# Performance work log

Hardware: AMD Instinct MI355X
Metric: run time of the kernel (lower is better)

The kernel has to match this reference:

```python
import jax, jax.numpy as jnp
import numpy as np

D_MODEL = 2048
NUM_HEADS = 16
HEAD_DIM = D_MODEL // NUM_HEADS
D_FF = 8192
EPS = 1e-6


def rmsnorm(x, w):
    return x * jax.lax.rsqrt(jnp.mean(x * x, axis=-1, keepdims=True) + EPS) * w


def setup_inputs() -> dict:
    key = jax.random.key(0)
    ks = jax.random.split(key, 8)
    B, S, D = 2, 2048, D_MODEL
    s = lambda d: 1.0 / np.sqrt(d)
    return {
        "x": jax.random.normal(ks[0], (B, S, D), dtype=jnp.float32),
        "w_qkv": jax.random.normal(ks[1], (D, 3 * D), dtype=jnp.float32) * s(D),
        "w_out": jax.random.normal(ks[2], (D, D), dtype=jnp.float32) * s(D),
        "w1": jax.random.normal(ks[3], (D, D_FF), dtype=jnp.float32) * s(D),
        "w2": jax.random.normal(ks[4], (D_FF, D), dtype=jnp.float32) * s(D_FF),
        "w3": jax.random.normal(ks[5], (D, D_FF), dtype=jnp.float32) * s(D),
        "g1": jnp.ones((D,), dtype=jnp.float32),
        "g2": jnp.ones((D,), dtype=jnp.float32),
    }


def attention(x, w_qkv, w_out):
    B, S, D = x.shape
    H, Hd = NUM_HEADS, HEAD_DIM
    qkv = (x @ w_qkv).reshape(B, S, 3, H, Hd)
    q = qkv[:, :, 0].transpose(0, 2, 1, 3)  # [B,H,S,Hd]
    k = qkv[:, :, 1].transpose(0, 2, 1, 3)
    v = qkv[:, :, 2].transpose(0, 2, 1, 3)
    scale = Hd ** -0.5
    attn = jnp.einsum("bhqd,bhkd->bhqk", q, k) * scale
    causal = jnp.tril(jnp.ones((S, S), dtype=bool))
    attn = jnp.where(causal, attn, -jnp.inf)
    attn = jax.nn.softmax(attn, axis=-1)
    out = jnp.einsum("bhqk,bhkd->bhqd", attn, v)
    out = out.transpose(0, 2, 1, 3).reshape(B, S, D)
    return out @ w_out


def ffn(x, w1, w2, w3):
    return (jax.nn.silu(x @ w1) * (x @ w3)) @ w2


def reference(x, w_qkv, w_out, w1, w2, w3, g1, g2):
    x = x + attention(rmsnorm(x, g1), w_qkv, w_out)
    return x + ffn(rmsnorm(x, g2), w1, w2, w3)
```

## Files before the change

### kernel.cpp

```cpp
#include <hip/hip_runtime.h>
#include <cstdint>
#include <cstddef>

typedef __bf16 bf16x8 __attribute__((ext_vector_type(8)));
typedef float f32x4 __attribute__((ext_vector_type(4)));

__device__ __forceinline__ void gl_lds16(const void* g, void* l) {
  __builtin_amdgcn_global_load_lds(
      (const __attribute__((address_space(1))) void*)g,
      (__attribute__((address_space(3))) void*)l, 16, 0, 0);
}

__global__ __launch_bounds__(256) void wconv_t_k(const float* __restrict__ W,
                                                 __bf16* __restrict__ WT,
                                                 int K, int N) {
  __shared__ float tile[32][33];
  const int c0 = blockIdx.x * 32, r0 = blockIdx.y * 32;
  const int tx = threadIdx.x & 31, ty = threadIdx.x >> 5;
#pragma unroll
  for (int i = 0; i < 32; i += 8)
    tile[ty + i][tx] = W[(size_t)(r0 + ty + i) * N + c0 + tx];
  __syncthreads();
#pragma unroll
  for (int i = 0; i < 32; i += 8)
    WT[(size_t)(c0 + ty + i) * K + r0 + tx] = (__bf16)tile[tx][ty + i];
}

__global__ __launch_bounds__(256) void rmsnorm_k(const float* __restrict__ x,
                                                 const float* __restrict__ g,
                                                 __bf16* __restrict__ out) {
  constexpr int D = 2048;
  const int row = blockIdx.x, t = threadIdx.x;
  const float4* xr = (const float4*)(x + (size_t)row * D);
  float4 a = xr[t * 2], b2 = xr[t * 2 + 1];
  float ss = a.x * a.x + a.y * a.y + a.z * a.z + a.w * a.w +
             b2.x * b2.x + b2.y * b2.y + b2.z * b2.z + b2.w * b2.w;
#pragma unroll
  for (int d = 1; d < 64; d <<= 1) ss += __shfl_xor(ss, d, 64);
  __shared__ float red[4];
  if ((t & 63) == 0) red[t >> 6] = ss;
  __syncthreads();
  float rs = rsqrtf((red[0] + red[1] + red[2] + red[3]) * (1.f / D) + 1e-6f);
  const float4* gr = (const float4*)g;
  float4 ga = gr[t * 2], gb = gr[t * 2 + 1];
  bf16x8 o8;
  o8[0] = (__bf16)(a.x * rs * ga.x);
  o8[1] = (__bf16)(a.y * rs * ga.y);
  o8[2] = (__bf16)(a.z * rs * ga.z);
  o8[3] = (__bf16)(a.w * rs * ga.w);
  o8[4] = (__bf16)(b2.x * rs * gb.x);
  o8[5] = (__bf16)(b2.y * rs * gb.y);
  o8[6] = (__bf16)(b2.z * rs * gb.z);
  o8[7] = (__bf16)(b2.w * rs * gb.w);
  *(bf16x8*)(out + (size_t)row * D + t * 8) = o8;
}

__global__ __launch_bounds__(256) void addrms_k(const float* __restrict__ p0,
                                                const float* __restrict__ p1,
                                                const float* __restrict__ res,
                                                const float* __restrict__ g,
                                                float* __restrict__ hout,
                                                __bf16* __restrict__ xnout) {
  constexpr int D = 2048;
  const int row = blockIdx.x, t = threadIdx.x;
  const size_t base = (size_t)row * D;
  float4 h[2];
#pragma unroll
  for (int j = 0; j < 2; ++j) {
    float4 a = ((const float4*)(p0 + base))[t * 2 + j];
    float4 b = ((const float4*)(p1 + base))[t * 2 + j];
    float4 c = ((const float4*)(res + base))[t * 2 + j];
    h[j].x = a.x + b.x + c.x; h[j].y = a.y + b.y + c.y;
    h[j].z = a.z + b.z + c.z; h[j].w = a.w + b.w + c.w;
    ((float4*)(hout + base))[t * 2 + j] = h[j];
  }
  float ss = h[0].x * h[0].x + h[0].y * h[0].y + h[0].z * h[0].z + h[0].w * h[0].w +
             h[1].x * h[1].x + h[1].y * h[1].y + h[1].z * h[1].z + h[1].w * h[1].w;
#pragma unroll
  for (int d = 1; d < 64; d <<= 1) ss += __shfl_xor(ss, d, 64);
  __shared__ float red[4];
  if ((t & 63) == 0) red[t >> 6] = ss;
  __syncthreads();
  float rs = rsqrtf((red[0] + red[1] + red[2] + red[3]) * (1.f / D) + 1e-6f);
  const float4* gr = (const float4*)g;
  float4 ga = gr[t * 2], gb = gr[t * 2 + 1];
  bf16x8 o8;
  o8[0] = (__bf16)(h[0].x * rs * ga.x);
  o8[1] = (__bf16)(h[0].y * rs * ga.y);
  o8[2] = (__bf16)(h[0].z * rs * ga.z);
  o8[3] = (__bf16)(h[0].w * rs * ga.w);
  o8[4] = (__bf16)(h[1].x * rs * gb.x);
  o8[5] = (__bf16)(h[1].y * rs * gb.y);
  o8[6] = (__bf16)(h[1].z * rs * gb.z);
  o8[7] = (__bf16)(h[1].w * rs * gb.w);
  *(bf16x8*)(xnout + base + t * 8) = o8;
}

__global__ __launch_bounds__(256) void addred_k(const float* __restrict__ p0,
                                                const float* __restrict__ p1,
                                                const float* __restrict__ res,
                                                float* __restrict__ out, int n4) {
  int i = blockIdx.x * 256 + threadIdx.x;
  const int stride = gridDim.x * 256;
  for (; i < n4; i += stride) {
    float4 a = ((const float4*)p0)[i];
    float4 b = ((const float4*)p1)[i];
    float4 c = ((const float4*)res)[i];
    float4 o = {a.x + b.x + c.x, a.y + b.y + c.y, a.z + b.z + c.z, a.w + b.w + c.w};
    ((float4*)out)[i] = o;
  }
}

#define RD_A(BUF, HALF) do {                                        \
  const __bf16* aT_ = &As[BUF][0] + aoff + (HALF) * 4096;           \
  _Pragma("unroll")                                                 \
  for (int mi = 0; mi < 4; ++mi) {                                  \
    Ar[mi][0] = *(const bf16x8*)(aT_ + mi * 1024 + k0off);          \
    Ar[mi][1] = *(const bf16x8*)(aT_ + mi * 1024 + k1off);          \
  } } while (0)

#define RD_B(BUF, NH) do {                                          \
  const __bf16* bT_ = &Bs[BUF][0] + boff + (NH) * 2048;             \
  _Pragma("unroll")                                                 \
  for (int ni = 0; ni < 2; ++ni) {                                  \
    Br[NH][ni][0] = *(const bf16x8*)(bT_ + ni * 1024 + k0off);      \
    Br[NH][ni][1] = *(const bf16x8*)(bT_ + ni * 1024 + k1off);      \
  } } while (0)

#define MQ(MH, NH) do {                                             \
  _Pragma("unroll")                                                 \
  for (int mi = 0; mi < 4; ++mi) {                                  \
    _Pragma("unroll")                                               \
    for (int ni = 0; ni < 2; ++ni) {                                \
      f32x4& a_ = acc[(MH) * 4 + mi][(NH) * 2 + ni];                \
      a_ = __builtin_amdgcn_mfma_f32_16x16x32_bf16(Ar[mi][0], Br[NH][ni][0], a_, 0, 0, 0); \
      a_ = __builtin_amdgcn_mfma_f32_16x16x32_bf16(Ar[mi][1], Br[NH][ni][1], a_, 0, 0, 0); \
    } } } while (0)

#define PH_MID() do {                                               \
  __builtin_amdgcn_sched_barrier(0);                                \
  __builtin_amdgcn_s_barrier();                                     \
  asm volatile("s_waitcnt lgkmcnt(0)" ::: "memory");                \
  __builtin_amdgcn_sched_barrier(0);                                \
  __builtin_amdgcn_s_setprio(1);                                    \
} while (0)

#define PH_END(VM) do {                                             \
  __builtin_amdgcn_s_setprio(0);                                    \
  asm volatile("s_waitcnt vmcnt(" #VM ")" ::: "memory");            \
  __builtin_amdgcn_sched_barrier(0);                                \
  __builtin_amdgcn_s_barrier();                                     \
} while (0)

#define PH_END_NOVM() do {                                          \
  __builtin_amdgcn_s_setprio(0);                                    \
  __builtin_amdgcn_s_barrier();                                     \
} while (0)

#define KTILE(BUF, STG0, STG1, STG2, STG3, END0, END1, END3) do {   \
  RD_A(BUF, 0); RD_B(BUF, 0); STG0; PH_MID(); MQ(0, 0); END0;       \
  RD_B(BUF, 1);               STG1; PH_MID(); MQ(0, 1); END1;       \
  RD_A(BUF, 1);               STG2; PH_MID(); MQ(1, 1); PH_END_NOVM(); \
                              STG3; PH_MID(); MQ(1, 0); END3;       \
} while (0)

template <int MODE>
__global__ __launch_bounds__(512, 2) void gemm8_k(
    const __bf16* __restrict__ A, const __bf16* __restrict__ BT,
    const float* __restrict__ res, const __bf16* __restrict__ aux,
    void* __restrict__ Cout, int M, int N, int K, int lda, int cswz) {
  __shared__ alignas(16) __bf16 As[2][256 * 64];
  __shared__ alignas(16) __bf16 Bs[2][256 * 64];
  const int tid = threadIdx.x;
  const int lane = tid & 63, w = tid >> 6;
  const int wm = w >> 2, wn = w & 3;
  const int l15 = lane & 15, l16 = lane >> 4;

  const int nbx = gridDim.x, nby = gridDim.y;
  const int nwg = nbx * nby;
  const int bid = blockIdx.y * nbx + blockIdx.x;
  const int swz = (bid & 7) * (nwg >> 3) + (bid >> 3);
  int bx, by;
  if (cswz) { by = swz % nby; bx = swz / nby; }
  else      { bx = swz % nbx; by = swz / nbx; }
  const int m0 = by * 256, n0 = bx * 256;
  const int nkt = K >> 6;

  float* CoutF = (float*)Cout;
  if constexpr (MODE == 4) {
    const int z = blockIdx.z;
    A += (size_t)z * K;
    BT += (size_t)z * K;
    CoutF += (size_t)z * M * N;
  }

  const int srow = tid >> 3;
  const int scole = ((tid & 7) * 8) ^ ((srow & 7) << 3);
  const int brow_i = ((tid >> 8) << 6) + ((tid >> 3) & 31);

  auto stgA = [&](int t, int h) {
    if (t < nkt) {
      char* dst = (char*)(&As[t & 1][0]) + h * 8192 + tid * 16;
      const __bf16* src = A + (size_t)(m0 + h * 64 + srow) * lda + t * 64 + scole;
      gl_lds16(src, dst);
      gl_lds16(src + (size_t)128 * lda, dst + 16384);
    }
  };
  auto stgB = [&](int t, int h) {
    if (t < nkt) {
      const int r = h * 32 + brow_i;
      char* dst = (char*)(&Bs[t & 1][0]) + r * 128 + (tid & 7) * 16;
      const __bf16* src = BT + (size_t)(n0 + r) * lda + t * 64 + scole;
      gl_lds16(src, dst);
      gl_lds16(src + (size_t)128 * lda, dst + 16384);
    }
  };

  const int rswz = (l15 & 7) << 3;
  const int k0off = (l16 * 8) ^ rswz;
  const int k1off = (32 + l16 * 8) ^ rswz;
  const int aoff = (wm * 128 + l15) * 64;
  const int boff = (wn * 64 + l15) * 64;

  f32x4 acc[8][4] = {};
  bf16x8 Ar[4][2], Br[2][2][2];

  stgA(0, 0); stgB(0, 0); stgB(0, 1); stgA(0, 1);
  stgA(1, 0); stgB(1, 0);
  asm volatile("s_waitcnt vmcnt(8)" ::: "memory");
  __builtin_amdgcn_s_barrier();

  int t = 0;
  for (; t + 3 < nkt; t += 2) {
    KTILE(0, stgB(t + 1, 1), stgA(t + 1, 1), stgA(t + 2, 0), stgB(t + 2, 0),
          PH_END(8), PH_END(8), PH_END(8));
    KTILE(1, stgB(t + 2, 1), stgA(t + 2, 1), stgA(t + 3, 0), stgB(t + 3, 0),
          PH_END(8), PH_END(8), PH_END(8));
  }
  KTILE(0, stgB(t + 1, 1), stgA(t + 1, 1), (void)0, (void)0,
        PH_END(8), PH_END(8), PH_END(4));
  KTILE(1, (void)0, (void)0, (void)0, (void)0,
        PH_END(2), PH_END(0), __builtin_amdgcn_s_setprio(0));

#pragma unroll
  for (int m = 0; m < 8; ++m) {
    const int rowb = m0 + wm * 128 + m * 16 + l16 * 4;
#pragma unroll
    for (int n = 0; n < 4; ++n) {
      const int col = n0 + wn * 64 + n * 16 + l15;
#pragma unroll
      for (int r = 0; r < 4; ++r) {
        const size_t idx = (size_t)(rowb + r) * N + col;
        float v = acc[m][n][r];
        if constexpr (MODE == 1) {
          CoutF[idx] = v + res[idx];
        } else if constexpr (MODE == 2) {
          float s = v / (1.f + __expf(-v));
          ((__bf16*)Cout)[idx] = (__bf16)s;
        } else if constexpr (MODE == 3) {
          ((__bf16*)Cout)[idx] = (__bf16)(v * (float)aux[idx]);
        } else if constexpr (MODE == 4) {
          CoutF[idx] = v;
        } else {
          ((__bf16*)Cout)[idx] = (__bf16)v;
        }
      }
    }
  }
}

__global__ __launch_bounds__(256) void vtrans_k(const __bf16* __restrict__ qkv,
                                                __bf16* __restrict__ VT) {
  constexpr int S = 2048;
  __shared__ __bf16 tile[64][65];
  const int s0 = blockIdx.x * 64, d0 = blockIdx.y * 64;
  const int bh = blockIdx.z, b = bh >> 4, h = bh & 15;
  const int tx = threadIdx.x & 63, ty = threadIdx.x >> 6;
  const size_t vbase = ((size_t)b * S * 3 + 2) * 2048 + h * 128;
#pragma unroll
  for (int i = 0; i < 16; ++i) {
    int s = ty + i * 4;
    tile[s][tx] = qkv[vbase + (size_t)(s0 + s) * 6144 + d0 + tx];
  }
  __syncthreads();
  const size_t obase = ((size_t)bh * 128 + d0) * S + s0;
#pragma unroll
  for (int i = 0; i < 16; ++i) {
    int d = ty + i * 4;
    VT[obase + (size_t)d * S + tx] = tile[tx][d];
  }
}

__global__ __launch_bounds__(512) void attn_k(const __bf16* __restrict__ qkv,
                                              const __bf16* __restrict__ VT,
                                              __bf16* __restrict__ out) {
  constexpr int S = 2048;
  const int bid = blockIdx.x;
  const int bh = (bid & 7) * 4 + ((bid >> 3) & 3);
  const int qb = 15 - (bid >> 5);
  const int b = bh >> 4, h = bh & 15;
  const int q0 = qb * 128;
  const int tid = threadIdx.x, lane = tid & 63, w = tid >> 6;
  const int l15 = lane & 15, l16 = lane >> 4;

  __shared__ __bf16 Ks[64 * 128];
  __shared__ __bf16 Vs[128 * 64];
  __shared__ __bf16 Ps[8][16 * 72];

  const size_t qbase = (size_t)b * S * 6144 + h * 128;
  const size_t kbase = qbase + 2048;
  const size_t vtbase = (size_t)bh * 128 * 2048;

  bf16x8 qf[4];
  {
    const __bf16* qp = qkv + qbase + (size_t)(q0 + w * 16 + l15) * 6144 + l16 * 8;
#pragma unroll
    for (int kc = 0; kc < 4; ++kc) qf[kc] = *(const bf16x8*)(qp + kc * 32);
  }

  f32x4 o[8] = {};
  float mrow[4] = {-1e30f, -1e30f, -1e30f, -1e30f};
  float lrow[4] = {0.f, 0.f, 0.f, 0.f};
  const float sm = 0.08838834764831845f * 1.4426950408889634f;

  int ksrow[2], kscol[2], vsrow[2], vscol[2];
#pragma unroll
  for (int c = 0; c < 2; ++c) {
    int P = (c * 512 + tid) * 16;
    int kr = P >> 8;
    ksrow[c] = kr;
    kscol[c] = ((P & 255) ^ ((kr & 7) << 4)) >> 1;
    int vr = P >> 7;
    vsrow[c] = vr;
    vscol[c] = ((P & 127) ^ ((vr & 7) << 4)) >> 1;
  }
  const int fswz = (l15 & 7) << 3;
  const int qrow_abs = q0 + w * 16 + l16 * 4;

#pragma unroll
  for (int c = 0; c < 2; ++c) {
    int e = (c * 512 + tid) * 8;
    gl_lds16(qkv + kbase + (size_t)ksrow[c] * 6144 + kscol[c], &Ks[e]);
    gl_lds16(VT + vtbase + (size_t)vsrow[c] * 2048 + vscol[c], &Vs[e]);
  }

  const int ntk = 2 * qb + 2;
  for (int kt = 0; kt < ntk; ++kt) {
    const int k0 = kt * 64;
    __syncthreads();

    bf16x8 kreg[2], vreg[2];
    const bool pf = kt + 1 < ntk;
    if (pf) {
      const int kn = k0 + 64;
#pragma unroll
      for (int c = 0; c < 2; ++c)
        kreg[c] = *(const bf16x8*)(qkv + kbase + (size_t)(kn + ksrow[c]) * 6144 + kscol[c]);
#pragma unroll
      for (int c = 0; c < 2; ++c)
        vreg[c] = *(const bf16x8*)(VT + vtbase + (size_t)vsrow[c] * 2048 + kn + vscol[c]);
    }

    f32x4 s4[4];
    __builtin_amdgcn_s_setprio(1);
#pragma unroll
    for (int f = 0; f < 4; ++f) {
      f32x4 accs = {};
#pragma unroll
      for (int kc = 0; kc < 4; ++kc) {
        bf16x8 kf = *(const bf16x8*)&Ks[(f * 16 + l15) * 128 + ((kc * 32 + l16 * 8) ^ fswz)];
        accs = __builtin_amdgcn_mfma_f32_16x16x32_bf16(qf[kc], kf, accs, 0, 0, 0);
      }
      s4[f] = accs;
    }
    __builtin_amdgcn_s_setprio(0);

    float pm[4] = {-1e30f, -1e30f, -1e30f, -1e30f};
    float pvv[4][4];
#pragma unroll
    for (int f = 0; f < 4; ++f) {
      const int key = k0 + f * 16 + l15;
#pragma unroll
      for (int r = 0; r < 4; ++r) {
        float s = s4[f][r] * sm;
        if (key > qrow_abs + r) s = -1e30f;
        pvv[f][r] = s;
        pm[r] = fmaxf(pm[r], s);
      }
    }
#pragma unroll
    for (int d = 1; d < 16; d <<= 1) {
#pragma unroll
      for (int r = 0; r < 4; ++r) pm[r] = fmaxf(pm[r], __shfl_xor(pm[r], d, 64));
    }
    float fac[4], ts[4];
#pragma unroll
    for (int r = 0; r < 4; ++r) {
      float mn = fmaxf(mrow[r], pm[r]);
      fac[r] = exp2f(mrow[r] - mn);
      mrow[r] = mn;
      ts[r] = 0.f;
    }
#pragma unroll
    for (int f = 0; f < 4; ++f) {
#pragma unroll
      for (int r = 0; r < 4; ++r) {
        float p = exp2f(pvv[f][r] - mrow[r]);
        ts[r] += p;
        Ps[w][(l16 * 4 + r) * 72 + f * 16 + l15] = (__bf16)p;
      }
    }
#pragma unroll
    for (int d = 1; d < 16; d <<= 1) {
#pragma unroll
      for (int r = 0; r < 4; ++r) ts[r] += __shfl_xor(ts[r], d, 64);
    }
#pragma unroll
    for (int r = 0; r < 4; ++r) lrow[r] = lrow[r] * fac[r] + ts[r];
#pragma unroll
    for (int n = 0; n < 8; ++n) {
      o[n][0] *= fac[0];
      o[n][1] *= fac[1];
      o[n][2] *= fac[2];
      o[n][3] *= fac[3];
    }
    __builtin_amdgcn_s_setprio(1);
#pragma unroll
    for (int kc = 0; kc < 2; ++kc) {
      bf16x8 pf2 = *(const bf16x8*)&Ps[w][l15 * 72 + kc * 32 + l16 * 8];
#pragma unroll
      for (int n = 0; n < 8; ++n) {
        bf16x8 vf = *(const bf16x8*)&Vs[(n * 16 + l15) * 64 + ((kc * 32 + l16 * 8) ^ fswz)];
        o[n] = __builtin_amdgcn_mfma_f32_16x16x32_bf16(pf2, vf, o[n], 0, 0, 0);
      }
    }
    __builtin_amdgcn_s_setprio(0);
    __syncthreads();

    if (pf) {
#pragma unroll
      for (int c = 0; c < 2; ++c) *(bf16x8*)&Ks[(c * 512 + tid) * 8] = kreg[c];
#pragma unroll
      for (int c = 0; c < 2; ++c) *(bf16x8*)&Vs[(c * 512 + tid) * 8] = vreg[c];
    }
  }

  const int orow = b * S + q0 + w * 16 + l16 * 4;
#pragma unroll
  for (int r = 0; r < 4; ++r) {
    const float inv = 1.f / lrow[r];
#pragma unroll
    for (int n = 0; n < 8; ++n)
      out[(size_t)(orow + r) * 2048 + h * 128 + n * 16 + l15] = (__bf16)(o[n][r] * inv);
  }
}

extern "C" void kernel_launch(void* const* d_in, const int* in_sizes, int n_in,
                              void* d_out, int out_size, void* d_ws, size_t ws_size,
                              hipStream_t stream) {
  (void)in_sizes; (void)n_in; (void)out_size; (void)ws_size;
  const float* x = (const float*)d_in[0];
  const float* w_qkv = (const float*)d_in[1];
  const float* w_out = (const float*)d_in[2];
  const float* w1 = (const float*)d_in[3];
  const float* w2 = (const float*)d_in[4];
  const float* w3 = (const float*)d_in[5];
  const float* g1 = (const float*)d_in[6];
  const float* g2 = (const float*)d_in[7];
  char* ws = (char*)d_ws;

  constexpr int Mr = 4096, D = 2048, DFF = 8192, TD = 6144;

  __bf16* wqkvT = (__bf16*)(ws + 0);
  __bf16* w1T   = (__bf16*)(ws + 0);
  __bf16* woutT = (__bf16*)(ws + 33554432);
  __bf16* qkvb  = (__bf16*)(ws + 41943040);
  __bf16* w3T   = (__bf16*)(ws + 41943040);
  __bf16* w2T   = (__bf16*)(ws + 75497472);
  __bf16* VTb   = (__bf16*)(ws + 92274688);
  __bf16* xn    = (__bf16*)(ws + 109051904);
  __bf16* attn  = (__bf16*)(ws + 125829120);
  float*  hbuf  = (float*)(ws + 142606336);
  __bf16* gbuf  = (__bf16*)(ws + 176160768);
  float*  pO    = (float*)(ws + 176160768);
  float*  pW0   = (float*)(ws + 0);

  wconv_t_k<<<dim3(TD / 32, D / 32), 256, 0, stream>>>(w_qkv, wqkvT, D, TD);
  wconv_t_k<<<dim3(D / 32, D / 32), 256, 0, stream>>>(w_out, woutT, D, D);
  rmsnorm_k<<<Mr, 256, 0, stream>>>(x, g1, xn);
  gemm8_k<0><<<dim3(TD / 256, Mr / 256), 512, 0, stream>>>(xn, wqkvT, nullptr, nullptr, qkvb, Mr, TD, D, D, 1);
  vtrans_k<<<dim3(32, 2, 32), 256, 0, stream>>>(qkvb, VTb);
  attn_k<<<512, 512, 0, stream>>>(qkvb, VTb, attn);
  gemm8_k<4><<<dim3(D / 256, Mr / 256, 2), 512, 0, stream>>>(attn, woutT, nullptr, nullptr, pO, Mr, D, D / 2, D, 0);
  addrms_k<<<Mr, 256, 0, stream>>>(pO, pO + (size_t)Mr * D, x, g2, hbuf, xn);
  wconv_t_k<<<dim3(DFF / 32, D / 32), 256, 0, stream>>>(w1, w1T, D, DFF);
  wconv_t_k<<<dim3(DFF / 32, D / 32), 256, 0, stream>>>(w3, w3T, D, DFF);
  wconv_t_k<<<dim3(D / 32, DFF / 32), 256, 0, stream>>>(w2, w2T, DFF, D);
  gemm8_k<2><<<dim3(DFF / 256, Mr / 256), 512, 0, stream>>>(xn, w1T, nullptr, nullptr, gbuf, Mr, DFF, D, D, 1);
  gemm8_k<3><<<dim3(DFF / 256, Mr / 256), 512, 0, stream>>>(xn, w3T, nullptr, gbuf, gbuf, Mr, DFF, D, D, 1);
  gemm8_k<4><<<dim3(D / 256, Mr / 256, 2), 512, 0, stream>>>(gbuf, w2T, nullptr, nullptr, pW0, Mr, D, DFF / 2, DFF, 0);
  addred_k<<<2048, 256, 0, stream>>>(pW0, pW0 + (size_t)Mr * D, hbuf, (float*)d_out, Mr * D / 4);
}
```

Baseline: 752.7 us.

## Restructure GEMM k-tile pipeline to issue LDS reads ahead of MFMA phases

Reorders each k-tile so LDS fragment reads for the next quadrant are issued before or between MFMA blocks rather than behind a barrier and lgkmcnt(0) wait. Global-to-LDS staging now follows the MFMAs, and the vmcnt thresholds are retuned. The explicit lgkmcnt waits are dropped, so the compiler must insert them. setprio now brackets only the MFMA loops. The aim is to overlap LDS latency with matrix math and cut stalls, at the cost of possible hazards from the changed wait counts and more register pressure from holding both B halves.

Result: faster. 737.0 us (-2.1%).

```diff
diff --git a/kernel.cpp b/kernel.cpp
--- a/kernel.cpp
+++ b/kernel.cpp
@@ -128,6 +128,7 @@
   } } while (0)
 
 #define MQ(MH, NH) do {                                             \
+  __builtin_amdgcn_s_setprio(1);                                    \
   _Pragma("unroll")                                                 \
   for (int mi = 0; mi < 4; ++mi) {                                  \
     _Pragma("unroll")                                               \
@@ -135,33 +136,29 @@
       f32x4& a_ = acc[(MH) * 4 + mi][(NH) * 2 + ni];                \
       a_ = __builtin_amdgcn_mfma_f32_16x16x32_bf16(Ar[mi][0], Br[NH][ni][0], a_, 0, 0, 0); \
       a_ = __builtin_amdgcn_mfma_f32_16x16x32_bf16(Ar[mi][1], Br[NH][ni][1], a_, 0, 0, 0); \
-    } } } while (0)
-
-#define PH_MID() do {                                               \
+    } }                                                             \
+  __builtin_amdgcn_s_setprio(0);                                    \
+} while (0)
+
+#define PEND(VM) do {                                               \
+  __builtin_amdgcn_sched_barrier(0);                                \
+  asm volatile("s_waitcnt vmcnt(" #VM ")" ::: "memory");            \
+  __builtin_amdgcn_s_barrier();                                     \
+  __builtin_amdgcn_sched_barrier(0);                                \
+} while (0)
+
+#define PEND_NOVM() do {                                            \
   __builtin_amdgcn_sched_barrier(0);                                \
   __builtin_amdgcn_s_barrier();                                     \
-  asm volatile("s_waitcnt lgkmcnt(0)" ::: "memory");                \
   __builtin_amdgcn_sched_barrier(0);                                \
-  __builtin_amdgcn_s_setprio(1);                                    \
 } while (0)
 
-#define PH_END(VM) do {                                             \
-  __builtin_amdgcn_s_setprio(0);                                    \
-  asm volatile("s_waitcnt vmcnt(" #VM ")" ::: "memory");            \
-  __builtin_amdgcn_sched_barrier(0);                                \
-  __builtin_amdgcn_s_barrier();                                     \
-} while (0)
-
-#define PH_END_NOVM() do {                                          \
-  __builtin_amdgcn_s_setprio(0);                                    \
-  __builtin_amdgcn_s_barrier();                                     \
-} while (0)
-
-#define KTILE(BUF, STG0, STG1, STG2, STG3, END0, END1, END3) do {   \
-  RD_A(BUF, 0); RD_B(BUF, 0); STG0; PH_MID(); MQ(0, 0); END0;       \
-  RD_B(BUF, 1);               STG1; PH_MID(); MQ(0, 1); END1;       \
-  RD_A(BUF, 1);               STG2; PH_MID(); MQ(1, 1); PH_END_NOVM(); \
-                              STG3; PH_MID(); MQ(1, 0); END3;       \
+#define KTILE(BUF, STG0, STG1, STG2, STG3, END0, END1, END2, END3) do { \
+  RD_A(BUF, 0); RD_B(BUF, 0); RD_B(BUF, 1);                         \
+  MQ(0, 0); STG0; END0;                                             \
+  MQ(0, 1); RD_A(BUF, 1); STG1; END1;                               \
+  MQ(1, 1); STG2; END2;                                             \
+  MQ(1, 0); STG3; END3;                                             \
 } while (0)
 
 template <int MODE>
@@ -227,20 +224,21 @@
 
   stgA(0, 0); stgB(0, 0); stgB(0, 1); stgA(0, 1);
   stgA(1, 0); stgB(1, 0);
-  asm volatile("s_waitcnt vmcnt(8)" ::: "memory");
+  asm volatile("s_waitcnt vmcnt(6)" ::: "memory");
   __builtin_amdgcn_s_barrier();
+  __builtin_amdgcn_sched_barrier(0);
 
   int t = 0;
   for (; t + 3 < nkt; t += 2) {
     KTILE(0, stgB(t + 1, 1), stgA(t + 1, 1), stgA(t + 2, 0), stgB(t + 2, 0),
-          PH_END(8), PH_END(8), PH_END(8));
+          PEND(6), PEND_NOVM(), PEND_NOVM(), PEND(6));
     KTILE(1, stgB(t + 2, 1), stgA(t + 2, 1), stgA(t + 3, 0), stgB(t + 3, 0),
-          PH_END(8), PH_END(8), PH_END(8));
+          PEND(6), PEND_NOVM(), PEND_NOVM(), PEND(6));
   }
   KTILE(0, stgB(t + 1, 1), stgA(t + 1, 1), (void)0, (void)0,
-        PH_END(8), PH_END(8), PH_END(4));
+        PEND(6), PEND_NOVM(), PEND_NOVM(), PEND(2));
   KTILE(1, (void)0, (void)0, (void)0, (void)0,
-        PH_END(2), PH_END(0), __builtin_amdgcn_s_setprio(0));
+        PEND(0), PEND_NOVM(), PEND_NOVM(), (void)0);
 
 #pragma unroll
   for (int m = 0; m < 8; ++m) {
```
